# Optimization experiments

Hardware: AMD Instinct MI355X
Metric: run time of the kernel (lower is better)

Reference implementation:

```python
import jax, jax.numpy as jnp
import numpy as np

B = 16; C = 20; M = 64
LEVELS = [("p3", 8, 128), ("p4", 16, 64), ("p5", 32, 32)]  # name, stride, H(=W)
BOUNDS = {"p3": (0.0, 64.0), "p4": (64.0, 128.0), "p5": (128.0, jnp.inf)}
TOPK = 1000; MAX_DET = 100; IOU_THR = 0.5; SCORE_THR = 0.3


def _grid(h, w, stride):
    # replicates get_fpn_location_coords (incl. torch's meshgrid(y, x) ordering)
    xs = stride * (jnp.arange(w, dtype=jnp.float32) + 0.5)
    ys = stride * (jnp.arange(h, dtype=jnp.float32) + 0.5)
    a, b = jnp.meshgrid(ys, xs, indexing="ij")
    return jnp.stack([a, b], axis=-1).reshape(h * w, 2)


def setup_inputs() -> dict:
    key = jax.random.key(0)
    ks = jax.random.split(key, 16)
    inp = {}
    inp["locs_p3"] = _grid(128, 128, 8)
    inp["locs_p4"] = _grid(64, 64, 16)
    inp["locs_p5"] = _grid(32, 32, 32)
    xy = jax.random.uniform(ks[0], (B, M, 2), minval=0.0, maxval=700.0)
    wh = jax.random.uniform(ks[1], (B, M, 2), minval=32.0, maxval=300.0)
    cid = jax.random.randint(ks[2], (B, M, 1), 0, C).astype(jnp.float32)
    gt = jnp.concatenate([xy, xy + wh, cid], axis=-1)
    pad = jnp.arange(M) >= (M - 16)  # last 16 rows are background padding
    inp["gt_boxes"] = jnp.where(pad[None, :, None], -1.0, gt)
    for i, (name, stride, h) in enumerate(LEVELS):
        n = h * h
        inp[f"cls_{name}"] = jax.random.normal(ks[3 + i], (B, n, C)) - 2.0
        inp[f"reg_{name}"] = jax.random.uniform(ks[6 + i], (B, n, 4), minval=0.0, maxval=8.0)
        inp[f"ctr_{name}"] = jax.random.normal(ks[9 + i], (B, n))
    return inp


def _match_level(centers, gt, lower, upper):
    # centers (N,2), gt (M,5) -> matched gt box per center (N,5), -1 for background
    x = centers[:, 0:1]; y = centers[:, 1:2]
    x0, y0, x1, y1 = gt[:, 0], gt[:, 1], gt[:, 2], gt[:, 3]
    ltrb = jnp.stack([x - x0[None], y - y0[None], x1[None] - x, y1[None] - y], axis=-1)  # (N,M,4)
    inside = ltrb.min(-1) > 0
    maxd = ltrb.max(-1)
    ok = inside & (maxd > lower) & (maxd < upper)
    areas = (x1 - x0) * (y1 - y0)
    quality = ok.astype(jnp.float32) * (1e8 - areas)[None, :]
    q = quality.max(-1)
    idx = jnp.argmax(quality, axis=-1)
    idx = jnp.where(q < 1e-5, -1, idx)
    matched = gt[jnp.clip(idx, 0)]
    return jnp.where((idx < 0)[:, None], -1.0, matched)


def _targets(centers, matched, stride):
    # fcos_get_deltas_from_locations + fcos_make_centerness_targets
    xc, yc = centers[:, 0], centers[:, 1]
    d = jnp.stack([(xc - matched[:, 0]) / stride, (yc - matched[:, 1]) / stride,
                   (matched[:, 2] - xc) / stride, (matched[:, 3] - yc) / stride], axis=1)
    bg = jnp.all(matched == -1.0, axis=1)
    d = jnp.where(bg[:, None], -1.0, d)
    l, t, r, b = d[:, 0], d[:, 1], d[:, 2], d[:, 3]
    ctr = jnp.sqrt(jnp.minimum(l, r) * jnp.minimum(t, b) / (jnp.maximum(l, r) * jnp.maximum(t, b)))
    ctr = jnp.where(jnp.all(d == -1.0, axis=1), -1.0, ctr)
    return d, ctr


def _decode(deltas, locs, stride):
    # fcos_apply_deltas_to_locations
    d = jnp.maximum(deltas, 0.0)
    xc, yc = locs[:, 0], locs[:, 1]
    return jnp.stack([xc - d[:, 0] * stride, yc - d[:, 1] * stride,
                      xc + d[:, 2] * stride, yc + d[:, 3] * stride], axis=1)


def _nms_keep(boxes, scores, valid):
    # sequential greedy NMS (argmax + IoU suppression), capped at MAX_DET picks
    areas = (boxes[:, 2] - boxes[:, 0]) * (boxes[:, 3] - boxes[:, 1])
    def body(_, state):
        active, keep = state
        s = jnp.where(active, scores, -jnp.inf)
        i = jnp.argmax(s)
        ok = s[i] > -jnp.inf
        b = boxes[i]
        xx1 = jnp.maximum(b[0], boxes[:, 0]); yy1 = jnp.maximum(b[1], boxes[:, 1])
        xx2 = jnp.minimum(b[2], boxes[:, 2]); yy2 = jnp.minimum(b[3], boxes[:, 3])
        inter = jnp.clip(xx2 - xx1, 0.0) * jnp.clip(yy2 - yy1, 0.0)
        iou = inter / (areas[i] + areas - inter)
        keep = keep.at[i].set(keep[i] | ok)
        active = jnp.where(ok, active & (iou <= IOU_THR), active)
        return active, keep
    _, keep = jax.lax.fori_loop(0, MAX_DET, body, (valid, jnp.zeros_like(valid)))
    return keep


def _infer_one(boxes, scores_cls):
    # boxes (N,4), scores_cls (N,C) -> masked detections (TOPK,5)
    score = scores_cls.max(-1)
    cls_id = jnp.argmax(scores_cls, axis=-1)
    sc, idx = jax.lax.top_k(score, TOPK)
    bx = boxes[idx]; cid = cls_id[idx]
    valid = sc > SCORE_THR
    max_coord = jnp.max(jnp.where(valid[:, None], bx, 0.0))
    off = cid.astype(bx.dtype) * (max_coord + 1.0)  # class_spec_nms offsets
    keep = _nms_keep(bx + off[:, None], sc, valid)
    det = jnp.concatenate([bx, sc[:, None]], axis=-1)
    return jnp.where(keep[:, None], det, 0.0)


def reference(locs_p3, locs_p4, locs_p5, gt_boxes, cls_p3, cls_p4, cls_p5,
              reg_p3, reg_p4, reg_p5, ctr_p3, ctr_p4, ctr_p5):
    locs = {"p3": locs_p3, "p4": locs_p4, "p5": locs_p5}
    cls = {"p3": cls_p3, "p4": cls_p4, "p5": cls_p5}
    reg = {"p3": reg_p3, "p4": reg_p4, "p5": reg_p5}
    ctr = {"p3": ctr_p3, "p4": ctr_p4, "p5": ctr_p5}
    # ---- training targets (no-grad in original) ----
    tgt_d, tgt_c = [], []
    for name, stride, _ in LEVELS:
        lo, hi = BOUNDS[name]
        matched = jax.vmap(lambda g, L=locs[name], lo=lo, hi=hi: _match_level(L, g, lo, hi))(gt_boxes)
        d, c = jax.vmap(lambda m, L=locs[name], s=stride: _targets(L, m, s))(matched)
        tgt_d.append(d); tgt_c.append(c)
    gt_deltas = jax.lax.stop_gradient(jnp.concatenate(tgt_d, axis=1))   # (B, N_total, 4)
    gt_ctr = jax.lax.stop_gradient(jnp.concatenate(tgt_c, axis=1))      # (B, N_total)
    # ---- inference: decode + score + class-specific NMS ----
    all_boxes, all_scores = [], []
    for name, stride, _ in LEVELS:
        bx = jax.vmap(lambda d, L=locs[name], s=stride: _decode(d, L, s))(reg[name])
        sc = jnp.sqrt(jax.nn.sigmoid(cls[name]) * jax.nn.sigmoid(ctr[name])[..., None])
        all_boxes.append(bx); all_scores.append(sc)
    boxes = jnp.concatenate(all_boxes, axis=1)    # (B, N_total, 4)
    scores = jnp.concatenate(all_scores, axis=1)  # (B, N_total, C)
    dets = jax.vmap(_infer_one)(boxes, scores)    # (B, TOPK, 5)
    return dets, gt_deltas, gt_ctr
```

## Files before the change

### kernel.cpp

```cpp
#include <hip/hip_runtime.h>
#include <hip/hip_bf16.h>
#include <math.h>
#include <stdint.h>

#pragma clang fp contract(off)

#define NB   16
#define NC   20
#define NM   64
#define NT   21504
#define OFF1 16384
#define OFF2 20480
#define TOPK 1000
#define DELTA_OFF 80000L
#define CTR_OFF   1456256L

#define WS_SCORES   0L
#define WS_BOXESW   344064L
#define WS_CIDW     1720320L
#define WS_TOPSC    2064384L
#define WS_TOPBOX   2080768L
#define WS_TOPSHIFT 2146304L
#define WS_TOPAREA  2211840L
#define WS_ACT      2228224L
#define WS_MATRIX   0L

__device__ __forceinline__ int detect_bf(const void* locs0) {
  unsigned w = *(const unsigned*)locs0;
  return ((w & 0xFFFFu) == 0u) ? 0 : 1;
}
__device__ __forceinline__ float ldin(const void* p, long i, int bf) {
  if (bf) return __uint_as_float(((unsigned)((const unsigned short*)p)[i]) << 16);
  return ((const float*)p)[i];
}
__device__ __forceinline__ unsigned short f2bf(float v) {
  unsigned w = __float_as_uint(v);
  return (unsigned short)((w + 0x7FFFu + ((w >> 16) & 1u)) >> 16);
}
__device__ __forceinline__ void stout(void* p, long i, float v, int bf) {
  if (bf) ((unsigned short*)p)[i] = f2bf(v);
  else    ((float*)p)[i] = v;
}

__global__ __launch_bounds__(256)
void k_main(const void* locs0, const void* locs1, const void* locs2,
            const void* gt,
            const void* cls0, const void* cls1, const void* cls2,
            const void* reg0, const void* reg1, const void* reg2,
            const void* ctr0, const void* ctr1, const void* ctr2,
            void* out, float* scores, float* boxesw, float* cidw) {
  __shared__ float sgt[NM * 5];
  const int bf  = detect_bf(locs0);
  const int b   = blockIdx.y;
  const int blk = blockIdx.x;
  const int tid = threadIdx.x;
  const int n   = blk * 256 + tid;

  const void *L, *CL, *RG, *CT; int NL, base; float stride, lower, upper;
  if (blk < 64)      { L=locs0; CL=cls0; RG=reg0; CT=ctr0; NL=16384; base=0;    stride=8.f;  lower=0.f;   upper=64.f; }
  else if (blk < 80) { L=locs1; CL=cls1; RG=reg1; CT=ctr1; NL=4096;  base=OFF1; stride=16.f; lower=64.f;  upper=128.f; }
  else               { L=locs2; CL=cls2; RG=reg2; CT=ctr2; NL=1024;  base=OFF2; stride=32.f; lower=128.f; upper=INFINITY; }
  const int nl = n - base;

  for (int i = tid; i < NM * 5; i += 256) sgt[i] = ldin(gt, (long)b * NM * 5 + i, bf);
  __syncthreads();

  float cx = ldin(L, (long)nl * 2 + 0, bf);
  float cy = ldin(L, (long)nl * 2 + 1, bf);

  float best = -1.0f; int bi = 0;
  for (int m = 0; m < NM; ++m) {
    float g0 = sgt[m*5+0], g1 = sgt[m*5+1], g2 = sgt[m*5+2], g3 = sgt[m*5+3];
    float l = cx - g0, t = cy - g1, r = g2 - cx, d = g3 - cy;
    float mn = fminf(fminf(l, t), fminf(r, d));
    float mx = fmaxf(fmaxf(l, t), fmaxf(r, d));
    bool  ok = (mn > 0.f) && (mx > lower) && (mx < upper);
    float area = (g2 - g0) * (g3 - g1);
    float q = ok ? (100000000.0f - area) : 0.f;
    if (q > best) { best = q; bi = m; }
  }
  float d0, d1, d2, d3, ctrv;
  if (best < 1e-5f) {
    d0 = d1 = d2 = d3 = -1.f; ctrv = -1.f;
  } else {
    float m0 = sgt[bi*5+0], m1 = sgt[bi*5+1], m2 = sgt[bi*5+2], m3 = sgt[bi*5+3];
    d0 = (cx - m0) / stride; d1 = (cy - m1) / stride;
    d2 = (m2 - cx) / stride; d3 = (m3 - cy) / stride;
    float mnlr = fminf(d0, d2), mntb = fminf(d1, d3);
    float mxlr = fmaxf(d0, d2), mxtb = fmaxf(d1, d3);
    ctrv = sqrtf((mnlr * mntb) / (mxlr * mxtb));
  }
  long dbase = DELTA_OFF + ((long)b * NT + n) * 4;
  if (!bf) {
    *(float4*)((float*)out + dbase) = make_float4(d0, d1, d2, d3);
  } else {
    ushort4 v; v.x = f2bf(d0); v.y = f2bf(d1); v.z = f2bf(d2); v.w = f2bf(d3);
    *(ushort4*)((unsigned short*)out + dbase) = v;
  }
  stout(out, CTR_OFF + (long)b * NT + n, ctrv, bf);

  float ct  = ldin(CT, (long)b * NL + nl, bf);
  float sct = 1.0f / (1.0f + expf(-ct));

  float cl[NC];
  long cb = ((long)b * NL + nl) * NC;
  if (!bf) {
    const float4* p = (const float4*)((const float*)CL + cb);
#pragma unroll
    for (int i = 0; i < 5; ++i) {
      float4 q = p[i];
      cl[4*i+0] = q.x; cl[4*i+1] = q.y; cl[4*i+2] = q.z; cl[4*i+3] = q.w;
    }
  } else {
    const uint2* p = (const uint2*)((const unsigned short*)CL + cb);
#pragma unroll
    for (int i = 0; i < 5; ++i) {
      uint2 q = p[i];
      cl[4*i+0] = __uint_as_float((q.x & 0xFFFFu) << 16);
      cl[4*i+1] = __uint_as_float(q.x & 0xFFFF0000u);
      cl[4*i+2] = __uint_as_float((q.y & 0xFFFFu) << 16);
      cl[4*i+3] = __uint_as_float(q.y & 0xFFFF0000u);
    }
  }
  float vmax = cl[0], v2 = -INFINITY; int ci = 0;
#pragma unroll
  for (int c = 1; c < NC; ++c) {
    if (cl[c] > vmax) { v2 = vmax; vmax = cl[c]; ci = c; }
    else if (cl[c] > v2) v2 = cl[c];
  }
  float smax;
  if (vmax - v2 < 1e-3f) {
    smax = -1.0f; ci = 0;
    for (int c = 0; c < NC; ++c) {
      float sv = 1.0f / (1.0f + expf(-cl[c]));
      float s  = sqrtf(sv * sct);
      if (s > smax) { smax = s; ci = c; }
    }
  } else {
    float sv = 1.0f / (1.0f + expf(-vmax));
    smax = sqrtf(sv * sct);
  }

  float r0, r1, r2, r3;
  long rbase = ((long)b * NL + nl) * 4;
  if (!bf) {
    float4 rv = *(const float4*)((const float*)RG + rbase);
    r0 = rv.x; r1 = rv.y; r2 = rv.z; r3 = rv.w;
  } else {
    uint2 rw = *(const uint2*)((const unsigned short*)RG + rbase);
    r0 = __uint_as_float((rw.x & 0xFFFFu) << 16); r1 = __uint_as_float(rw.x & 0xFFFF0000u);
    r2 = __uint_as_float((rw.y & 0xFFFFu) << 16); r3 = __uint_as_float(rw.y & 0xFFFF0000u);
  }
  r0 = fmaxf(r0, 0.f); r1 = fmaxf(r1, 0.f); r2 = fmaxf(r2, 0.f); r3 = fmaxf(r3, 0.f);
  long o = (long)b * NT + n;
  scores[o] = smax;
  *(float4*)(boxesw + o * 4) =
      make_float4(cx - r0 * stride, cy - r1 * stride, cx + r2 * stride, cy + r3 * stride);
  cidw[o] = (float)ci;
}

__device__ __forceinline__ unsigned wscan(unsigned v, int lane) {
  for (int off = 1; off < 64; off <<= 1) {
    unsigned u = __shfl_up(v, off);
    if (lane >= off) v += u;
  }
  return v;
}

__global__ __launch_bounds__(1024)
void k_select(const float* scores, const float* boxesw, const float* cidw,
              float* topScore, float* topBox, float* topShift, float* topArea,
              unsigned long long* actInit) {
  const int b    = blockIdx.x;
  const int tid  = threadIdx.x;
  const int wid  = tid >> 6;
  const int lane = tid & 63;
  const float* sb = scores + (long)b * NT;

  __shared__ unsigned hist[8192];
  unsigned long long* selKeys = (unsigned long long*)hist;
  __shared__ unsigned wsum[16];
  __shared__ unsigned sTop, sBefore, sSub, selCnt;
  __shared__ float redf[16];
  __shared__ float sMaxC;

  unsigned inv[21];
#pragma unroll
  for (int k = 0; k < 21; ++k)
    inv[k] = ~__float_as_uint(sb[tid + k * 1024]);

  for (int i = tid; i < 8192; i += 1024) hist[i] = 0u;
  __syncthreads();
#pragma unroll
  for (int k = 0; k < 21; ++k)
    atomicAdd(&hist[(inv[k] >> 17) - 0x6000u], 1u);
  __syncthreads();
  {
    unsigned hloc[8], s0 = 0;
#pragma unroll
    for (int j = 0; j < 8; ++j) { hloc[j] = hist[8 * tid + j]; s0 += hloc[j]; }
    unsigned sc = wscan(s0, lane);
    if (lane == 63) wsum[wid] = sc;
    __syncthreads();
    unsigned basev = 0;
    for (int w = 0; w < wid; ++w) basev += wsum[w];
    unsigned cumBefore = basev + sc - s0;
    if (cumBefore < TOPK && cumBefore + s0 >= TOPK) {
      unsigned c = cumBefore;
#pragma unroll
      for (int j = 0; j < 8; ++j) {
        if (c + hloc[j] >= TOPK) { sTop = (8 * tid + j) + 0x6000u; sBefore = c; break; }
        c += hloc[j];
      }
    }
  }
  __syncthreads();
  const unsigned topBits = sTop;
  const unsigned r = TOPK - sBefore;

  for (int i = tid; i < 8192; i += 1024) hist[i] = 0u;
  __syncthreads();
#pragma unroll
  for (int k = 0; k < 21; ++k)
    if ((inv[k] >> 17) == topBits) atomicAdd(&hist[(inv[k] >> 4) & 0x1FFFu], 1u);
  __syncthreads();
  {
    unsigned hloc[8], s0 = 0;
#pragma unroll
    for (int j = 0; j < 8; ++j) { hloc[j] = hist[8 * tid + j]; s0 += hloc[j]; }
    unsigned sc = wscan(s0, lane);
    if (lane == 63) wsum[wid] = sc;
    __syncthreads();
    unsigned basev = 0;
    for (int w = 0; w < wid; ++w) basev += wsum[w];
    unsigned cumBefore = basev + sc - s0;
    if (cumBefore < r && cumBefore + s0 >= r) {
      unsigned c = cumBefore;
#pragma unroll
      for (int j = 0; j < 8; ++j) {
        if (c + hloc[j] >= r) { sSub = 8 * tid + j; break; }
        c += hloc[j];
      }
    }
  }
  __syncthreads();
  const unsigned long long cutEnd =
      ((unsigned long long)topBits << 17) | ((unsigned long long)(sSub + 1u) << 4);
  if (tid == 0) selCnt = 0u;
  __syncthreads();

#pragma unroll
  for (int k = 0; k < 21; ++k)
    if ((unsigned long long)inv[k] < cutEnd) {
      unsigned p = atomicAdd(&selCnt, 1u);
      if (p < 1024u) selKeys[p] = ((unsigned long long)inv[k] << 32) | (unsigned)(tid + k * 1024);
    }
  __syncthreads();
  unsigned total = selCnt < 1024u ? selCnt : 1024u;
  unsigned long long key =
      ((unsigned)tid < total) ? selKeys[tid] : 0xFFFFFFFFFFFFFFFFull;
  __syncthreads();

  for (unsigned k = 2; k <= 1024; k <<= 1) {
    for (unsigned j = k >> 1; j > 0; j >>= 1) {
      unsigned long long other;
      if (j >= 64) {
        selKeys[tid] = key; __syncthreads();
        other = selKeys[tid ^ j]; __syncthreads();
      } else {
        other = __shfl(key, (int)(lane ^ j));
      }
      bool up = ((tid & k) == 0);
      bool takeMin = (((tid & j) == 0) == up);
      key = takeMin ? (key < other ? key : other) : (key > other ? key : other);
    }
  }

  float sc = __uint_as_float(~(unsigned)(key >> 32));
  float4 bv = make_float4(0.f, 0.f, 0.f, 0.f);
  float cid = 0.f;
  if (tid < TOPK) {
    long o = (long)b * NT + (unsigned)key;
    bv = *(const float4*)(boxesw + o * 4);
    cid = cidw[o];
  } else sc = 0.f;

  float loc = (tid < TOPK)
      ? ((sc > 0.3f) ? fmaxf(fmaxf(bv.x, bv.y), fmaxf(bv.z, bv.w)) : 0.0f)
      : -INFINITY;
  for (int o = 32; o > 0; o >>= 1) loc = fmaxf(loc, __shfl_down(loc, o));
  if (lane == 0) redf[wid] = loc;
  __syncthreads();
  if (tid == 0) {
    float m = redf[0];
    for (int w = 1; w < 16; ++w) m = fmaxf(m, redf[w]);
    sMaxC = m;
  }
  __syncthreads();

  float offm = sMaxC + 1.0f;
  long tb = (long)b * 1024 + tid;
  if (tid < TOPK) {
    float o4 = cid * offm;
    float s0 = bv.x + o4, s1 = bv.y + o4, s2 = bv.z + o4, s3 = bv.w + o4;
    *(float4*)(topShift + tb * 4) = make_float4(s0, s1, s2, s3);
    topArea[tb]  = (s2 - s0) * (s3 - s1);
    *(float4*)(topBox + tb * 4) = bv;
    topScore[tb] = sc;
  } else {
    *(float4*)(topShift + tb * 4) = make_float4(0.f, 0.f, 0.f, 0.f);
    topArea[tb]  = 0.f;
    *(float4*)(topBox + tb * 4) = make_float4(0.f, 0.f, 0.f, 0.f);
    topScore[tb] = 0.f;
  }
  unsigned long long vb = __ballot((tid < TOPK) && (sc > 0.3f));
  if (lane == 0) actInit[b * 16 + wid] = vb;
}

__global__ __launch_bounds__(1024)
void k_iou(const float* topShift, const float* topArea, unsigned* matrix) {
  const int wh  = blockIdx.x;
  const int b   = blockIdx.y;
  const int tid = threadIdx.x;
  const int jbase = (wh >> 1) * 64 + (wh & 1) * 32;
  __shared__ float jx0[32], jy0[32], jx1[32], jy1[32], ja[32];
  if (tid < 32) {
    long tj = (long)b * 1024 + jbase + tid;
    float4 s = *(const float4*)(topShift + tj * 4);
    jx0[tid] = s.x; jy0[tid] = s.y; jx1[tid] = s.z; jy1[tid] = s.w;
    ja[tid] = topArea[tj];
  }
  __syncthreads();
  if (tid > jbase + 31) return;
  long ti = (long)b * 1024 + tid;
  float4 si = *(const float4*)(topShift + ti * 4);
  float ai  = topArea[ti];
  unsigned word = 0u;
  for (int k = 0; k < 32; ++k) {
    float xx1 = fmaxf(si.x, jx0[k]);
    float yy1 = fmaxf(si.y, jy0[k]);
    float xx2 = fminf(si.z, jx1[k]);
    float yy2 = fminf(si.w, jy1[k]);
    float inter = fmaxf(xx2 - xx1, 0.f) * fmaxf(yy2 - yy1, 0.f);
    float iou = inter / (ai + ja[k] - inter);
    if (!(iou <= 0.5f)) word |= (1u << k);
  }
  matrix[ti * 32 + wh] = word;
}

__global__ __launch_bounds__(256)
void k_scan(const unsigned long long* matrix, const unsigned long long* actInit,
            const float* topBox, const float* topScore, void* out, const void* locs0) {
  const int bf   = detect_bf(locs0);
  const int b    = blockIdx.x;
  const int tid  = threadIdx.x;
  const int wid  = tid >> 6;
  const int lane = tid & 63;
  const unsigned long long* M = matrix + (long)b * 1024 * 16;

  __shared__ unsigned long long rows[2][64][16];
  __shared__ unsigned long long keepSh[16];

  unsigned long long act = 0ull, keep = 0ull;
  if (wid == 0 && lane < 16) act = actInit[b * 16 + lane];

  for (int t = tid; t < 1024; t += 256)
    rows[0][t >> 4][t & 15] = M[t];
  __syncthreads();

  int kept = 0;
  for (int c = 0; c < 16; ++c) {
    if (wid > 0) {
      if (c < 15) {
        for (int t = tid - 64; t < 1024; t += 192)
          rows[(c + 1) & 1][t >> 4][t & 15] = M[(long)(c + 1) * 1024 + t];
      }
    } else {
      unsigned long long cur = __shfl(act, c);
      while (cur && kept < 100) {
        int k = __ffsll((unsigned long long)cur) - 1;
        ++kept;
        if (lane == c) keep |= (1ull << k);
        unsigned long long rrow = (lane < 16) ? rows[c & 1][k][lane] : 0ull;
        act &= ~rrow;
        cur = __shfl(act, c);
      }
    }
    __syncthreads();
  }
  if (wid == 0 && lane < 16) keepSh[lane] = keep;
  __syncthreads();

  for (int r = tid; r < TOPK; r += 256) {
    bool kp = (keepSh[r >> 6] >> (r & 63)) & 1ull;
    long tb = (long)b * 1024 + r;
    float4 bx = *(const float4*)(topBox + tb * 4);
    float sc  = topScore[tb];
    long o = ((long)b * TOPK + r) * 5;
    stout(out, o + 0, kp ? bx.x : 0.f, bf);
    stout(out, o + 1, kp ? bx.y : 0.f, bf);
    stout(out, o + 2, kp ? bx.z : 0.f, bf);
    stout(out, o + 3, kp ? bx.w : 0.f, bf);
    stout(out, o + 4, kp ? sc   : 0.f, bf);
  }
}

extern "C" void kernel_launch(void* const* d_in, const int* in_sizes, int n_in,
                              void* d_out, int out_size, void* d_ws, size_t ws_size,
                              hipStream_t stream) {
  const void* locs0 = d_in[0];
  const void* locs1 = d_in[1];
  const void* locs2 = d_in[2];
  const void* gt    = d_in[3];

  int ic[3], ir[3], it[3];
  if (n_in >= 13 && in_sizes[5] == 16 * 4096 * 20) {
    ic[0]=4; ic[1]=5; ic[2]=6;  ir[0]=7; ir[1]=8; ir[2]=9;  it[0]=10; it[1]=11; it[2]=12;
  } else {
    ic[0]=4; ic[1]=7; ic[2]=10; ir[0]=5; ir[1]=8; ir[2]=11; it[0]=6;  it[1]=9;  it[2]=12;
  }
  const void* cls0 = d_in[ic[0]]; const void* cls1 = d_in[ic[1]]; const void* cls2 = d_in[ic[2]];
  const void* reg0 = d_in[ir[0]]; const void* reg1 = d_in[ir[1]]; const void* reg2 = d_in[ir[2]];
  const void* ctr0 = d_in[it[0]]; const void* ctr1 = d_in[it[1]]; const void* ctr2 = d_in[it[2]];

  float* ws       = (float*)d_ws;
  float* scores   = ws + WS_SCORES;
  float* boxesw   = ws + WS_BOXESW;
  float* cidw     = ws + WS_CIDW;
  float* topScore = ws + WS_TOPSC;
  float* topBox   = ws + WS_TOPBOX;
  float* topShift = ws + WS_TOPSHIFT;
  float* topArea  = ws + WS_TOPAREA;
  unsigned long long* actInit = (unsigned long long*)(ws + WS_ACT);
  unsigned*           matrix32 = (unsigned*)(ws + WS_MATRIX);
  unsigned long long* matrix64 = (unsigned long long*)(ws + WS_MATRIX);

  k_main<<<dim3(NT / 256, NB), 256, 0, stream>>>(locs0, locs1, locs2, gt,
                                                 cls0, cls1, cls2,
                                                 reg0, reg1, reg2,
                                                 ctr0, ctr1, ctr2,
                                                 d_out, scores, boxesw, cidw);
  k_select<<<NB, 1024, 0, stream>>>(scores, boxesw, cidw,
                                    topScore, topBox, topShift, topArea, actInit);
  k_iou<<<dim3(32, NB), 1024, 0, stream>>>(topShift, topArea, matrix32);
  k_scan<<<NB, 256, 0, stream>>>(matrix64, actInit, topBox, topScore, d_out, locs0);
}
```

Before: 186.3 us.

## Fuse top-k selection, IoU matrix and NMS scan into one per-image kernel

Merges the select, IoU and scan kernels into a single per-image block that keeps shifted boxes and areas in shared memory and computes only the upper-triangular IoU words. This removes two launches and the global round trips for the top-k buffers. The greedy scan now reads suppression rows directly from global memory with volatile loads instead of LDS-prefetched rows, which adds serial load latency, and the IoU work runs on only one block per image.

```diff
diff --git a/kernel.cpp b/kernel.cpp
--- a/kernel.cpp
+++ b/kernel.cpp
@@ -18,12 +18,7 @@
 #define WS_SCORES   0L
 #define WS_BOXESW   344064L
 #define WS_CIDW     1720320L
-#define WS_TOPSC    2064384L
-#define WS_TOPBOX   2080768L
-#define WS_TOPSHIFT 2146304L
-#define WS_TOPAREA  2211840L
-#define WS_ACT      2228224L
-#define WS_MATRIX   0L
+#define WS_MATRIX   2064384L
 
 __device__ __forceinline__ int detect_bf(const void* locs0) {
   unsigned w = *(const unsigned*)locs0;
@@ -168,9 +163,9 @@
 }
 
 __global__ __launch_bounds__(1024)
-void k_select(const float* scores, const float* boxesw, const float* cidw,
-              float* topScore, float* topBox, float* topShift, float* topArea,
-              unsigned long long* actInit) {
+void k_post(const float* scores, const float* boxesw, const float* cidw,
+            unsigned* matrix32, void* out, const void* locs0) {
+  const int bf   = detect_bf(locs0);
   const int b    = blockIdx.x;
   const int tid  = threadIdx.x;
   const int wid  = tid >> 6;
@@ -179,10 +174,13 @@
 
   __shared__ unsigned hist[8192];
   unsigned long long* selKeys = (unsigned long long*)hist;
+  __shared__ float shiftS[4096];
+  __shared__ float areaS[1024];
   __shared__ unsigned wsum[16];
   __shared__ unsigned sTop, sBefore, sSub, selCnt;
   __shared__ float redf[16];
   __shared__ float sMaxC;
+  __shared__ unsigned long long actSh[16], keepSh[16];
 
   unsigned inv[21];
 #pragma unroll
@@ -299,108 +297,74 @@
   __syncthreads();
 
   float offm = sMaxC + 1.0f;
-  long tb = (long)b * 1024 + tid;
   if (tid < TOPK) {
     float o4 = cid * offm;
     float s0 = bv.x + o4, s1 = bv.y + o4, s2 = bv.z + o4, s3 = bv.w + o4;
-    *(float4*)(topShift + tb * 4) = make_float4(s0, s1, s2, s3);
-    topArea[tb]  = (s2 - s0) * (s3 - s1);
-    *(float4*)(topBox + tb * 4) = bv;
-    topScore[tb] = sc;
-  } else {
-    *(float4*)(topShift + tb * 4) = make_float4(0.f, 0.f, 0.f, 0.f);
-    topArea[tb]  = 0.f;
-    *(float4*)(topBox + tb * 4) = make_float4(0.f, 0.f, 0.f, 0.f);
-    topScore[tb] = 0.f;
+    *(float4*)(shiftS + tid * 4) = make_float4(s0, s1, s2, s3);
+    areaS[tid] = (s2 - s0) * (s3 - s1);
+  } else {
+    *(float4*)(shiftS + tid * 4) = make_float4(0.f, 0.f, 0.f, 0.f);
+    areaS[tid] = 0.f;
   }
   unsigned long long vb = __ballot((tid < TOPK) && (sc > 0.3f));
-  if (lane == 0) actInit[b * 16 + wid] = vb;
-}
-
-__global__ __launch_bounds__(1024)
-void k_iou(const float* topShift, const float* topArea, unsigned* matrix) {
-  const int wh  = blockIdx.x;
-  const int b   = blockIdx.y;
-  const int tid = threadIdx.x;
-  const int jbase = (wh >> 1) * 64 + (wh & 1) * 32;
-  __shared__ float jx0[32], jy0[32], jx1[32], jy1[32], ja[32];
-  if (tid < 32) {
-    long tj = (long)b * 1024 + jbase + tid;
-    float4 s = *(const float4*)(topShift + tj * 4);
-    jx0[tid] = s.x; jy0[tid] = s.y; jx1[tid] = s.z; jy1[tid] = s.w;
-    ja[tid] = topArea[tj];
-  }
-  __syncthreads();
-  if (tid > jbase + 31) return;
-  long ti = (long)b * 1024 + tid;
-  float4 si = *(const float4*)(topShift + ti * 4);
-  float ai  = topArea[ti];
-  unsigned word = 0u;
-  for (int k = 0; k < 32; ++k) {
-    float xx1 = fmaxf(si.x, jx0[k]);
-    float yy1 = fmaxf(si.y, jy0[k]);
-    float xx2 = fminf(si.z, jx1[k]);
-    float yy2 = fminf(si.w, jy1[k]);
-    float inter = fmaxf(xx2 - xx1, 0.f) * fmaxf(yy2 - yy1, 0.f);
-    float iou = inter / (ai + ja[k] - inter);
-    if (!(iou <= 0.5f)) word |= (1u << k);
-  }
-  matrix[ti * 32 + wh] = word;
-}
-
-__global__ __launch_bounds__(256)
-void k_scan(const unsigned long long* matrix, const unsigned long long* actInit,
-            const float* topBox, const float* topScore, void* out, const void* locs0) {
-  const int bf   = detect_bf(locs0);
-  const int b    = blockIdx.x;
-  const int tid  = threadIdx.x;
-  const int wid  = tid >> 6;
-  const int lane = tid & 63;
-  const unsigned long long* M = matrix + (long)b * 1024 * 16;
-
-  __shared__ unsigned long long rows[2][64][16];
-  __shared__ unsigned long long keepSh[16];
-
-  unsigned long long act = 0ull, keep = 0ull;
-  if (wid == 0 && lane < 16) act = actInit[b * 16 + lane];
-
-  for (int t = tid; t < 1024; t += 256)
-    rows[0][t >> 4][t & 15] = M[t];
-  __syncthreads();
-
-  int kept = 0;
-  for (int c = 0; c < 16; ++c) {
-    if (wid > 0) {
-      if (c < 15) {
-        for (int t = tid - 64; t < 1024; t += 192)
-          rows[(c + 1) & 1][t >> 4][t & 15] = M[(long)(c + 1) * 1024 + t];
+  if (lane == 0) { actSh[wid] = vb; keepSh[wid] = 0ull; }
+  __syncthreads();
+
+  {
+    const float4* shiftF4 = (const float4*)shiftS;
+    int wh2 = 0;
+    for (int p = tid; p < 16896; p += 1024) {
+      while (16 * (wh2 + 1) * (wh2 + 2) <= p) ++wh2;
+      int i = p - 16 * wh2 * (wh2 + 1);
+      float4 si = shiftF4[i];
+      float ai  = areaS[i];
+      int jbase = wh2 * 32;
+      unsigned word = 0u;
+      for (int k = 0; k < 32; ++k) {
+        float4 sj = shiftF4[jbase + k];
+        float xx1 = fmaxf(si.x, sj.x);
+        float yy1 = fmaxf(si.y, sj.y);
+        float xx2 = fminf(si.z, sj.z);
+        float yy2 = fminf(si.w, sj.w);
+        float inter = fmaxf(xx2 - xx1, 0.f) * fmaxf(yy2 - yy1, 0.f);
+        float iou = inter / (ai + areaS[jbase + k] - inter);
+        if (!(iou <= 0.5f)) word |= (1u << k);
       }
-    } else {
+      matrix32[((long)b * 1024 + i) * 32 + wh2] = word;
+    }
+  }
+  __threadfence();
+  __syncthreads();
+
+  if (wid == 0) {
+    const volatile unsigned long long* M64 =
+        (const volatile unsigned long long*)matrix32 + (long)b * 1024 * 16;
+    unsigned long long act = (lane < 16) ? actSh[lane] : 0ull;
+    unsigned long long keep = 0ull;
+    int kept = 0;
+    for (int c = 0; c < 16 && kept < 100; ++c) {
       unsigned long long cur = __shfl(act, c);
       while (cur && kept < 100) {
-        int k = __ffsll((unsigned long long)cur) - 1;
+        int k = __ffsll(cur) - 1;
+        int idx = c * 64 + k;
         ++kept;
         if (lane == c) keep |= (1ull << k);
-        unsigned long long rrow = (lane < 16) ? rows[c & 1][k][lane] : 0ull;
-        act &= ~rrow;
+        unsigned long long row = (lane < 16) ? M64[(long)idx * 16 + lane] : 0ull;
+        act &= ~row;
         cur = __shfl(act, c);
       }
     }
-    __syncthreads();
-  }
-  if (wid == 0 && lane < 16) keepSh[lane] = keep;
-  __syncthreads();
-
-  for (int r = tid; r < TOPK; r += 256) {
-    bool kp = (keepSh[r >> 6] >> (r & 63)) & 1ull;
-    long tb = (long)b * 1024 + r;
-    float4 bx = *(const float4*)(topBox + tb * 4);
-    float sc  = topScore[tb];
-    long o = ((long)b * TOPK + r) * 5;
-    stout(out, o + 0, kp ? bx.x : 0.f, bf);
-    stout(out, o + 1, kp ? bx.y : 0.f, bf);
-    stout(out, o + 2, kp ? bx.z : 0.f, bf);
-    stout(out, o + 3, kp ? bx.w : 0.f, bf);
+    if (lane < 16) keepSh[lane] = keep;
+  }
+  __syncthreads();
+
+  if (tid < TOPK) {
+    bool kp = (keepSh[tid >> 6] >> (tid & 63)) & 1ull;
+    long o = ((long)b * TOPK + tid) * 5;
+    stout(out, o + 0, kp ? bv.x : 0.f, bf);
+    stout(out, o + 1, kp ? bv.y : 0.f, bf);
+    stout(out, o + 2, kp ? bv.z : 0.f, bf);
+    stout(out, o + 3, kp ? bv.w : 0.f, bf);
     stout(out, o + 4, kp ? sc   : 0.f, bf);
   }
 }
@@ -427,21 +391,12 @@
   float* scores   = ws + WS_SCORES;
   float* boxesw   = ws + WS_BOXESW;
   float* cidw     = ws + WS_CIDW;
-  float* topScore = ws + WS_TOPSC;
-  float* topBox   = ws + WS_TOPBOX;
-  float* topShift = ws + WS_TOPSHIFT;
-  float* topArea  = ws + WS_TOPAREA;
-  unsigned long long* actInit = (unsigned long long*)(ws + WS_ACT);
-  unsigned*           matrix32 = (unsigned*)(ws + WS_MATRIX);
-  unsigned long long* matrix64 = (unsigned long long*)(ws + WS_MATRIX);
+  unsigned* matrix32 = (unsigned*)(ws + WS_MATRIX);
 
   k_main<<<dim3(NT / 256, NB), 256, 0, stream>>>(locs0, locs1, locs2, gt,
                                                  cls0, cls1, cls2,
                                                  reg0, reg1, reg2,
                                                  ctr0, ctr1, ctr2,
                                                  d_out, scores, boxesw, cidw);
-  k_select<<<NB, 1024, 0, stream>>>(scores, boxesw, cidw,
-                                    topScore, topBox, topShift, topArea, actInit);
-  k_iou<<<dim3(32, NB), 1024, 0, stream>>>(topShift, topArea, matrix32);
-  k_scan<<<NB, 256, 0, stream>>>(matrix64, actInit, topBox, topScore, d_out, locs0);
-}
+  k_post<<<NB, 1024, 0, stream>>>(scores, boxesw, cidw, matrix32, d_out, locs0);
+}
```

Measured after the change: 284.6 us. 52.8% more time.

## Fuse IoU-matrix and NMS scan kernels using a last-block-done counter

Applied to the files above, without the earlier changes.

Merges the IoU bitmask kernel and the greedy NMS scan kernel into one launch. Each block writes its slice of the suppression matrix, fences, then bumps a per-image atomic counter; the block that finishes last runs the scan and writes the output. The counters are reset in k_select, and the matrix moves to its own workspace region instead of aliasing the scores buffer. This removes one kernel launch and its inter-kernel gap, at the cost of extra fences and atomics, and the scan now runs inside a 1024-thread block with a larger shared-memory footprint.

```diff
diff --git a/kernel.cpp b/kernel.cpp
--- a/kernel.cpp
+++ b/kernel.cpp
@@ -23,7 +23,8 @@
 #define WS_TOPSHIFT 2146304L
 #define WS_TOPAREA  2211840L
 #define WS_ACT      2228224L
-#define WS_MATRIX   0L
+#define WS_CNT      2228736L
+#define WS_MATRIX   2229248L
 
 __device__ __forceinline__ int detect_bf(const void* locs0) {
   unsigned w = *(const unsigned*)locs0;
@@ -170,7 +171,7 @@
 __global__ __launch_bounds__(1024)
 void k_select(const float* scores, const float* boxesw, const float* cidw,
               float* topScore, float* topBox, float* topShift, float* topArea,
-              unsigned long long* actInit) {
+              unsigned long long* actInit, unsigned* counters) {
   const int b    = blockIdx.x;
   const int tid  = threadIdx.x;
   const int wid  = tid >> 6;
@@ -183,6 +184,8 @@
   __shared__ unsigned sTop, sBefore, sSub, selCnt;
   __shared__ float redf[16];
   __shared__ float sMaxC;
+
+  if (tid == 0) counters[b] = 0u;
 
   unsigned inv[21];
 #pragma unroll
@@ -318,12 +321,23 @@
 }
 
 __global__ __launch_bounds__(1024)
-void k_iou(const float* topShift, const float* topArea, unsigned* matrix) {
-  const int wh  = blockIdx.x;
-  const int b   = blockIdx.y;
-  const int tid = threadIdx.x;
-  const int jbase = (wh >> 1) * 64 + (wh & 1) * 32;
+void k_iou_scan(const float* topShift, const float* topArea,
+                const float* topBox, const float* topScore,
+                unsigned* matrix32, unsigned* counters,
+                const unsigned long long* actInit,
+                void* out, const void* locs0) {
+  const int wh   = blockIdx.x;
+  const int b    = blockIdx.y;
+  const int tid  = threadIdx.x;
+  const int wid  = tid >> 6;
+  const int lane = tid & 63;
+  const int jbase = wh * 32;
+
   __shared__ float jx0[32], jy0[32], jx1[32], jy1[32], ja[32];
+  __shared__ unsigned long long rows[2][64][16];
+  __shared__ unsigned long long keepSh[16];
+  __shared__ int sLast;
+
   if (tid < 32) {
     long tj = (long)b * 1024 + jbase + tid;
     float4 s = *(const float4*)(topShift + tj * 4);
@@ -331,40 +345,37 @@
     ja[tid] = topArea[tj];
   }
   __syncthreads();
-  if (tid > jbase + 31) return;
-  long ti = (long)b * 1024 + tid;
-  float4 si = *(const float4*)(topShift + ti * 4);
-  float ai  = topArea[ti];
-  unsigned word = 0u;
-  for (int k = 0; k < 32; ++k) {
-    float xx1 = fmaxf(si.x, jx0[k]);
-    float yy1 = fmaxf(si.y, jy0[k]);
-    float xx2 = fminf(si.z, jx1[k]);
-    float yy2 = fminf(si.w, jy1[k]);
-    float inter = fmaxf(xx2 - xx1, 0.f) * fmaxf(yy2 - yy1, 0.f);
-    float iou = inter / (ai + ja[k] - inter);
-    if (!(iou <= 0.5f)) word |= (1u << k);
-  }
-  matrix[ti * 32 + wh] = word;
-}
-
-__global__ __launch_bounds__(256)
-void k_scan(const unsigned long long* matrix, const unsigned long long* actInit,
-            const float* topBox, const float* topScore, void* out, const void* locs0) {
-  const int bf   = detect_bf(locs0);
-  const int b    = blockIdx.x;
-  const int tid  = threadIdx.x;
-  const int wid  = tid >> 6;
-  const int lane = tid & 63;
-  const unsigned long long* M = matrix + (long)b * 1024 * 16;
-
-  __shared__ unsigned long long rows[2][64][16];
-  __shared__ unsigned long long keepSh[16];
+  if (tid <= jbase + 31) {
+    long ti = (long)b * 1024 + tid;
+    float4 si = *(const float4*)(topShift + ti * 4);
+    float ai  = topArea[ti];
+    unsigned word = 0u;
+    for (int k = 0; k < 32; ++k) {
+      float xx1 = fmaxf(si.x, jx0[k]);
+      float yy1 = fmaxf(si.y, jy0[k]);
+      float xx2 = fminf(si.z, jx1[k]);
+      float yy2 = fminf(si.w, jy1[k]);
+      float inter = fmaxf(xx2 - xx1, 0.f) * fmaxf(yy2 - yy1, 0.f);
+      float iou = inter / (ai + ja[k] - inter);
+      if (!(iou <= 0.5f)) word |= (1u << k);
+    }
+    matrix32[((long)b * 1024 + tid) * 32 + wh] = word;
+  }
+
+  __syncthreads();
+  __threadfence();
+  if (tid == 0) sLast = (atomicAdd(&counters[b], 1u) == 31u);
+  __syncthreads();
+  if (!sLast) return;
+  __threadfence();
+
+  const volatile unsigned long long* M =
+      (const volatile unsigned long long*)matrix32 + (long)b * 1024 * 16;
 
   unsigned long long act = 0ull, keep = 0ull;
   if (wid == 0 && lane < 16) act = actInit[b * 16 + lane];
 
-  for (int t = tid; t < 1024; t += 256)
+  for (int t = tid; t < 1024; t += 1024)
     rows[0][t >> 4][t & 15] = M[t];
   __syncthreads();
 
@@ -372,13 +383,13 @@
   for (int c = 0; c < 16; ++c) {
     if (wid > 0) {
       if (c < 15) {
-        for (int t = tid - 64; t < 1024; t += 192)
+        for (int t = tid - 64; t < 1024; t += 960)
           rows[(c + 1) & 1][t >> 4][t & 15] = M[(long)(c + 1) * 1024 + t];
       }
     } else {
       unsigned long long cur = __shfl(act, c);
       while (cur && kept < 100) {
-        int k = __ffsll((unsigned long long)cur) - 1;
+        int k = __ffsll(cur) - 1;
         ++kept;
         if (lane == c) keep |= (1ull << k);
         unsigned long long rrow = (lane < 16) ? rows[c & 1][k][lane] : 0ull;
@@ -391,12 +402,13 @@
   if (wid == 0 && lane < 16) keepSh[lane] = keep;
   __syncthreads();
 
-  for (int r = tid; r < TOPK; r += 256) {
-    bool kp = (keepSh[r >> 6] >> (r & 63)) & 1ull;
-    long tb = (long)b * 1024 + r;
+  const int bf = detect_bf(locs0);
+  if (tid < TOPK) {
+    bool kp = (keepSh[tid >> 6] >> (tid & 63)) & 1ull;
+    long tb = (long)b * 1024 + tid;
     float4 bx = *(const float4*)(topBox + tb * 4);
     float sc  = topScore[tb];
-    long o = ((long)b * TOPK + r) * 5;
+    long o = ((long)b * TOPK + tid) * 5;
     stout(out, o + 0, kp ? bx.x : 0.f, bf);
     stout(out, o + 1, kp ? bx.y : 0.f, bf);
     stout(out, o + 2, kp ? bx.z : 0.f, bf);
@@ -431,9 +443,9 @@
   float* topBox   = ws + WS_TOPBOX;
   float* topShift = ws + WS_TOPSHIFT;
   float* topArea  = ws + WS_TOPAREA;
-  unsigned long long* actInit = (unsigned long long*)(ws + WS_ACT);
+  unsigned long long* actInit  = (unsigned long long*)(ws + WS_ACT);
+  unsigned*           counters = (unsigned*)(ws + WS_CNT);
   unsigned*           matrix32 = (unsigned*)(ws + WS_MATRIX);
-  unsigned long long* matrix64 = (unsigned long long*)(ws + WS_MATRIX);
 
   k_main<<<dim3(NT / 256, NB), 256, 0, stream>>>(locs0, locs1, locs2, gt,
                                                  cls0, cls1, cls2,
@@ -441,7 +453,10 @@
                                                  ctr0, ctr1, ctr2,
                                                  d_out, scores, boxesw, cidw);
   k_select<<<NB, 1024, 0, stream>>>(scores, boxesw, cidw,
-                                    topScore, topBox, topShift, topArea, actInit);
-  k_iou<<<dim3(32, NB), 1024, 0, stream>>>(topShift, topArea, matrix32);
-  k_scan<<<NB, 256, 0, stream>>>(matrix64, actInit, topBox, topScore, d_out, locs0);
-}
+                                    topScore, topBox, topShift, topArea,
+                                    actInit, counters);
+  k_iou_scan<<<dim3(32, NB), 1024, 0, stream>>>(topShift, topArea,
+                                                topBox, topScore,
+                                                matrix32, counters, actInit,
+                                                d_out, locs0);
+}
```

New measurement: 395.1 us. 2.12x slower.
